# Optimization experiments

Measured on AMD Instinct MI355X. Metric: run time of the kernel, lower is better.

## Reference

```python
import jax, jax.numpy as jnp
import numpy as np

NUM_VALUES = 32000
EMB = 512
BATCH = 2048
SEQ = 64


def setup_inputs() -> dict:
    key = jax.random.key(0)
    ks = jax.random.split(key, 6)
    s = 1.0 / np.sqrt(EMB)  # torch LSTMCell init scale
    x = jax.random.randint(ks[0], (BATCH, SEQ), 0, NUM_VALUES, dtype=jnp.int64)
    emb = jax.random.normal(ks[1], (NUM_VALUES, EMB), dtype=jnp.float32)
    W_ih = jax.random.uniform(ks[2], (4 * EMB, EMB), jnp.float32, -s, s)
    W_hh = jax.random.uniform(ks[3], (4 * EMB, EMB), jnp.float32, -s, s)
    b_ih = jax.random.uniform(ks[4], (4 * EMB,), jnp.float32, -s, s)
    b_hh = jax.random.uniform(ks[5], (4 * EMB,), jnp.float32, -s, s)
    return {"x": x, "emb": emb, "W_ih": W_ih, "W_hh": W_hh, "b_ih": b_ih, "b_hh": b_hh}


def _lstm_cell(h, c, xt, W_ih, W_hh, b):
    # gates layout (torch): [i, f, g, o] along first axis of 4E
    gates = xt @ W_ih.T + h @ W_hh.T + b  # [B, 4E]
    i, f, g, o = jnp.split(gates, 4, axis=-1)
    i = jax.nn.sigmoid(i)
    f = jax.nn.sigmoid(f)
    g = jnp.tanh(g)
    o = jax.nn.sigmoid(o)
    c = f * c + i * g
    h = o * jnp.tanh(c)
    return h, c


def reference(x, emb, W_ih, W_hh, b_ih, b_hh):
    B, S = x.shape
    E = emb.shape[1]
    xe = emb[x.T]  # [S, B, E] (transpose(0,1) then embedding)
    b = b_ih + b_hh
    h0 = jnp.zeros((B, E), dtype=emb.dtype)
    c0 = jnp.zeros((B, E), dtype=emb.dtype)

    def step(carry, xt):
        h, c = carry
        h, c = _lstm_cell(h, c, xt, W_ih, W_hh, b)
        return (h, c), None

    (h, _), _ = jax.lax.scan(step, (h0, c0), xe)
    return h
```

## Files before the change

### kernel.cpp

```cpp
#include <hip/hip_runtime.h>
#include <hip/hip_bf16.h>

#define B_   2048
#define E_   512
#define S_   64
#define K_   1024
#define NG   2048

#define BM 128
#define BN 128
#define BK 64
#define ND  4

typedef __attribute__((ext_vector_type(8))) short  bfrag8;
typedef __attribute__((ext_vector_type(4))) float  f32x4;

#define WAITVM(N) asm volatile("s_waitcnt vmcnt(" #N ")" ::: "memory")
#define SBAR() do { __builtin_amdgcn_s_barrier(); __builtin_amdgcn_sched_barrier(0); } while (0)

__device__ __forceinline__ void gload16(const void* g, void* l) {
  __builtin_amdgcn_global_load_lds(
      (const __attribute__((address_space(1))) unsigned int*)g,
      (__attribute__((address_space(3))) unsigned int*)l,
      16, 0, 0);
}

__device__ __forceinline__ float sigm(float x)      { return 1.f / (1.f + __expf(-x)); }
__device__ __forceinline__ float tanh_fast(float x) { return 2.f / (1.f + __expf(-2.f * x)) - 1.f; }

__global__ __launch_bounds__(256) void prep_weights(
    const float* __restrict__ Wih, const float* __restrict__ Whh,
    const float* __restrict__ bih, const float* __restrict__ bhh,
    __hip_bfloat16* __restrict__ Wp, float* __restrict__ biasP)
{
  int p  = blockIdx.x;
  int te = p >> 7;
  int c  = p & 127;
  int hi = (c >> 6) & 1;
  int g  = (c >> 4) & 3;
  int q  = c & 15;
  int e  = te * 32 + hi * 16 + q;
  int n  = g * E_ + e;
  const float* s0 = Wih + (size_t)n * E_;
  const float* s1 = Whh + (size_t)n * E_;
  __hip_bfloat16* dst = Wp + (size_t)p * K_;
  for (int k = threadIdx.x; k < E_; k += 256) {
    dst[k]       = __float2bfloat16(s0[k]);
    dst[E_ + k]  = __float2bfloat16(s1[k]);
  }
  if (threadIdx.x == 0) biasP[p] = bih[n] + bhh[n];
}

__global__ __launch_bounds__(256) void init_state(
    const int* __restrict__ x, const float* __restrict__ emb,
    float* __restrict__ c, __hip_bfloat16* __restrict__ A0)
{
  int b  = blockIdx.x;
  int xi = x[(size_t)b * S_ + 0];
  const float* e = emb + (size_t)xi * E_;
  __hip_bfloat16* a = A0 + (size_t)b * K_;
  float* cr = c + (size_t)b * E_;
  for (int k = threadIdx.x; k < E_; k += 256) {
    a[k]       = __float2bfloat16(e[k]);
    a[E_ + k]  = __float2bfloat16(0.f);
    cr[k]      = 0.f;
  }
}

__global__ __launch_bounds__(512, 1) void lstm_step(
    const __hip_bfloat16* __restrict__ Acur,
    __hip_bfloat16* __restrict__ Anext,
    const __hip_bfloat16* __restrict__ Wp,
    const float* __restrict__ biasP,
    float* __restrict__ c,
    const int* __restrict__ x,
    const float* __restrict__ emb,
    float* __restrict__ out,
    int t)
{
  __shared__ __hip_bfloat16 As[ND][BM * BK];
  __shared__ __hip_bfloat16 Bs[ND][BN * BK];

  const int tid = threadIdx.x;
  const int x7 = blockIdx.x & 7;
  const int i  = blockIdx.x >> 3;
  const int tm = (x7 & 1) * 8 + (i & 7);
  const int te = (x7 >> 1) * 4 + (i >> 3);

  const int w  = tid >> 6, l = tid & 63;
  const int wr = w >> 1;
  const int wc = w & 1;
  const int lq = l & 15, lh = l >> 4;

  const int arow0 = tm * BM;
  const int brow0 = te * BN;
  const int e     = te * 32 + wc * 16 + lq;

  float bg[4];
#pragma unroll
  for (int n = 0; n < 4; ++n)
    bg[n] = biasP[te * 128 + wc * 64 + n * 16 + lq];

  float cold[2][4];
  int   xiv[2][4];
  const int tn = (t < S_ - 1) ? t + 1 : S_ - 1;
#pragma unroll
  for (int m = 0; m < 2; ++m)
#pragma unroll
    for (int r = 0; r < 4; ++r) {
      int b = arow0 + wr * 32 + m * 16 + lh * 4 + r;
      cold[m][r] = c[(size_t)b * E_ + e];
      xiv[m][r]  = x[(size_t)b * S_ + tn];
    }
  __builtin_amdgcn_sched_barrier(0);

  auto stageA = [&](int kt, int buf) {
    const int k0 = kt * BK;
#pragma unroll
    for (int it = 0; it < 2; ++it) {
      int ch  = it * 512 + tid;
      int cl  = ch ^ ((ch >> 3) & 7);
      int row = cl >> 3, gr = cl & 7;
      gload16(Acur + (size_t)(arow0 + row) * K_ + k0 + gr * 8, &As[buf][ch * 8]);
    }
  };
  auto stageB = [&](int kt, int buf) {
    const int k0 = kt * BK;
#pragma unroll
    for (int it = 0; it < 2; ++it) {
      int ch  = it * 512 + tid;
      int cl  = ch ^ ((ch >> 3) & 7);
      int row = cl >> 3, gr = cl & 7;
      gload16(Wp + (size_t)(brow0 + row) * K_ + k0 + gr * 8, &Bs[buf][ch * 8]);
    }
  };

  stageA(0, 0); stageB(0, 0);
  stageA(1, 1); stageB(1, 1);
  stageA(2, 2); stageB(2, 2);
  __builtin_amdgcn_sched_barrier(0);

  float ev[2][4];
#pragma unroll
  for (int m = 0; m < 2; ++m)
#pragma unroll
    for (int r = 0; r < 4; ++r)
      ev[m][r] = emb[(size_t)xiv[m][r] * E_ + e];
  __builtin_amdgcn_sched_barrier(0);

  int aoff[2][2], boff[2][4];
#pragma unroll
  for (int ks = 0; ks < 2; ++ks) {
#pragma unroll
    for (int m = 0; m < 2; ++m) {
      int cl = (wr * 32 + m * 16 + lq) * 8 + ks * 4 + lh;
      aoff[ks][m] = (cl ^ ((cl >> 3) & 7)) * 8;
    }
#pragma unroll
    for (int n = 0; n < 4; ++n) {
      int cl = (wc * 64 + n * 16 + lq) * 8 + ks * 4 + lh;
      boff[ks][n] = (cl ^ ((cl >> 3) & 7)) * 8;
    }
  }

  f32x4 acc[2][4];
#pragma unroll
  for (int m = 0; m < 2; ++m)
#pragma unroll
    for (int n = 0; n < 4; ++n)
      acc[m][n] = (f32x4){0.f, 0.f, 0.f, 0.f};

  auto mfma_iter = [&](int rb) {
    const __hip_bfloat16* Ab = &As[rb][0];
    const __hip_bfloat16* Bb = &Bs[rb][0];
#pragma unroll
    for (int ks = 0; ks < 2; ++ks) {
      bfrag8 af[2], bfr[4];
#pragma unroll
      for (int m = 0; m < 2; ++m) af[m]  = *(const bfrag8*)(Ab + aoff[ks][m]);
#pragma unroll
      for (int n = 0; n < 4; ++n) bfr[n] = *(const bfrag8*)(Bb + boff[ks][n]);
      __builtin_amdgcn_s_setprio(1);
#pragma unroll
      for (int m = 0; m < 2; ++m)
#pragma unroll
        for (int n = 0; n < 4; ++n)
          acc[m][n] = __builtin_amdgcn_mfma_f32_16x16x32_bf16(af[m], bfr[n], acc[m][n], 0, 0, 0);
      __builtin_amdgcn_s_setprio(0);
    }
  };

  WAITVM(16); SBAR(); stageA(3, 3);  stageB(3, 3);  mfma_iter(0);
  WAITVM(16); SBAR(); stageA(4, 0);  stageB(4, 0);  mfma_iter(1);
  WAITVM(16); SBAR(); stageA(5, 1);  stageB(5, 1);  mfma_iter(2);
  WAITVM(8);  SBAR(); stageA(6, 2);  stageB(6, 2);  mfma_iter(3);
#pragma unroll 1
  for (int kt = 4; kt <= 12; ++kt) {
    WAITVM(8); SBAR();
    stageA(kt + 3, (kt + 3) & 3); stageB(kt + 3, (kt + 3) & 3);
    mfma_iter(kt & 3);
  }
  WAITVM(8); SBAR(); mfma_iter(1);
  WAITVM(4); SBAR(); mfma_iter(2);
  WAITVM(0); SBAR(); mfma_iter(3);

  const bool last = (t == S_ - 1);
#pragma unroll
  for (int m = 0; m < 2; ++m) {
#pragma unroll
    for (int r = 0; r < 4; ++r) {
      int b = arow0 + wr * 32 + m * 16 + lh * 4 + r;
      float iv = acc[m][0][r] + bg[0];
      float fv = acc[m][1][r] + bg[1];
      float gv = acc[m][2][r] + bg[2];
      float ov = acc[m][3][r] + bg[3];
      size_t cidx = (size_t)b * E_ + e;
      float ig = sigm(iv), fg = sigm(fv), gg = tanh_fast(gv), og = sigm(ov);
      float cn = fg * cold[m][r] + ig * gg;
      c[cidx] = cn;
      float h = og * tanh_fast(cn);
      if (last) {
        out[cidx] = h;
      } else {
        Anext[(size_t)b * K_ + E_ + e] = __float2bfloat16(h);
        Anext[(size_t)b * K_ + e]      = __float2bfloat16(ev[m][r]);
      }
    }
  }
}

extern "C" void kernel_launch(void* const* d_in, const int* in_sizes, int n_in,
                              void* d_out, int out_size, void* d_ws, size_t ws_size,
                              hipStream_t stream) {
  const int*   x   = (const int*)d_in[0];
  const float* emb = (const float*)d_in[1];
  const float* Wih = (const float*)d_in[2];
  const float* Whh = (const float*)d_in[3];
  const float* bih = (const float*)d_in[4];
  const float* bhh = (const float*)d_in[5];
  float* out = (float*)d_out;
  (void)in_sizes; (void)n_in; (void)out_size; (void)ws_size;

  char* p = (char*)d_ws;
  __hip_bfloat16* Wp    = (__hip_bfloat16*)p;  p += (size_t)NG * K_ * 2;
  float*          biasP = (float*)p;           p += (size_t)NG * 4;
  float*          c     = (float*)p;           p += (size_t)B_ * E_ * 4;
  __hip_bfloat16* A0    = (__hip_bfloat16*)p;  p += (size_t)B_ * K_ * 2;
  __hip_bfloat16* A1    = (__hip_bfloat16*)p;  p += (size_t)B_ * K_ * 2;

  prep_weights<<<NG, 256, 0, stream>>>(Wih, Whh, bih, bhh, Wp, biasP);
  init_state<<<B_, 256, 0, stream>>>(x, emb, c, A0);
  for (int t = 0; t < S_; ++t) {
    __hip_bfloat16* Ac = (t & 1) ? A1 : A0;
    __hip_bfloat16* An = (t & 1) ? A0 : A1;
    lstm_step<<<256, 512, 0, stream>>>(Ac, An, Wp, biasP, c, x, emb, out, t);
  }
}
```

Baseline: 1.220 ms.

## Pregather all embeddings upfront and split A operand into Xe and H buffers

Replaces the per-step embedding gather (scattered fp32 loads of emb for the next timestep inside each lstm_step) with a single pregather kernel that writes all timesteps' embeddings as bf16 into a [S,B,E] buffer. The step kernel now streams its A tile from Xe for the first half of K and from a compact H buffer for the second half. Loads of bias and old cell state are moved from the prologue into the middle of the K loop to hide their latency. The cost is a 128MB workspace buffer and an extra upfront gather pass.

```diff
diff --git a/kernel.cpp b/kernel.cpp
--- a/kernel.cpp
+++ b/kernel.cpp
@@ -51,30 +51,32 @@
   if (threadIdx.x == 0) biasP[p] = bih[n] + bhh[n];
 }
 
-__global__ __launch_bounds__(256) void init_state(
+__global__ __launch_bounds__(256) void pregather(
     const int* __restrict__ x, const float* __restrict__ emb,
-    float* __restrict__ c, __hip_bfloat16* __restrict__ A0)
+    __hip_bfloat16* __restrict__ Xe)
 {
-  int b  = blockIdx.x;
-  int xi = x[(size_t)b * S_ + 0];
-  const float* e = emb + (size_t)xi * E_;
-  __hip_bfloat16* a = A0 + (size_t)b * K_;
-  float* cr = c + (size_t)b * E_;
-  for (int k = threadIdx.x; k < E_; k += 256) {
-    a[k]       = __float2bfloat16(e[k]);
-    a[E_ + k]  = __float2bfloat16(0.f);
-    cr[k]      = 0.f;
-  }
+  int row  = blockIdx.x * 4 + (threadIdx.x >> 6);
+  int lane = threadIdx.x & 63;
+  int b = row >> 6, t = row & 63;
+  size_t xi = (size_t)x[row];
+  const float* src = emb + xi * E_ + lane * 8;
+  float4 f0 = *(const float4*)(src);
+  float4 f1 = *(const float4*)(src + 4);
+  union { __hip_bfloat16 h[8]; uint4 v; } u;
+  u.h[0] = __float2bfloat16(f0.x); u.h[1] = __float2bfloat16(f0.y);
+  u.h[2] = __float2bfloat16(f0.z); u.h[3] = __float2bfloat16(f0.w);
+  u.h[4] = __float2bfloat16(f1.x); u.h[5] = __float2bfloat16(f1.y);
+  u.h[6] = __float2bfloat16(f1.z); u.h[7] = __float2bfloat16(f1.w);
+  *(uint4*)(Xe + ((size_t)t * B_ + b) * E_ + lane * 8) = u.v;
 }
 
 __global__ __launch_bounds__(512, 1) void lstm_step(
-    const __hip_bfloat16* __restrict__ Acur,
-    __hip_bfloat16* __restrict__ Anext,
+    const __hip_bfloat16* __restrict__ Xe,
+    const __hip_bfloat16* __restrict__ Hp,
+    __hip_bfloat16* __restrict__ Hn,
     const __hip_bfloat16* __restrict__ Wp,
     const float* __restrict__ biasP,
     float* __restrict__ c,
-    const int* __restrict__ x,
-    const float* __restrict__ emb,
     float* __restrict__ out,
     int t)
 {
@@ -96,36 +98,20 @@
   const int brow0 = te * BN;
   const int e     = te * 32 + wc * 16 + lq;
 
-  float bg[4];
-#pragma unroll
-  for (int n = 0; n < 4; ++n)
-    bg[n] = biasP[te * 128 + wc * 64 + n * 16 + lq];
-
-  float cold[2][4];
-  int   xiv[2][4];
-  const int tn = (t < S_ - 1) ? t + 1 : S_ - 1;
-#pragma unroll
-  for (int m = 0; m < 2; ++m)
-#pragma unroll
-    for (int r = 0; r < 4; ++r) {
-      int b = arow0 + wr * 32 + m * 16 + lh * 4 + r;
-      cold[m][r] = c[(size_t)b * E_ + e];
-      xiv[m][r]  = x[(size_t)b * S_ + tn];
-    }
-  __builtin_amdgcn_sched_barrier(0);
-
-  auto stageA = [&](int kt, int buf) {
-    const int k0 = kt * BK;
+  auto stageA = [&](int tt, int buf) {
 #pragma unroll
     for (int it = 0; it < 2; ++it) {
       int ch  = it * 512 + tid;
       int cl  = ch ^ ((ch >> 3) & 7);
       int row = cl >> 3, gr = cl & 7;
-      gload16(Acur + (size_t)(arow0 + row) * K_ + k0 + gr * 8, &As[buf][ch * 8]);
+      const __hip_bfloat16* src = (tt < 8)
+        ? Xe + ((size_t)t * B_ + arow0 + row) * E_ + tt * 64 + gr * 8
+        : Hp + (size_t)(arow0 + row) * E_ + (tt - 8) * 64 + gr * 8;
+      gload16(src, &As[buf][ch * 8]);
     }
   };
-  auto stageB = [&](int kt, int buf) {
-    const int k0 = kt * BK;
+  auto stageB = [&](int tt, int buf) {
+    const int k0 = tt * BK;
 #pragma unroll
     for (int it = 0; it < 2; ++it) {
       int ch  = it * 512 + tid;
@@ -140,14 +126,6 @@
   stageA(2, 2); stageB(2, 2);
   __builtin_amdgcn_sched_barrier(0);
 
-  float ev[2][4];
-#pragma unroll
-  for (int m = 0; m < 2; ++m)
-#pragma unroll
-    for (int r = 0; r < 4; ++r)
-      ev[m][r] = emb[(size_t)xiv[m][r] * E_ + e];
-  __builtin_amdgcn_sched_barrier(0);
-
   int aoff[2][2], boff[2][4];
 #pragma unroll
   for (int ks = 0; ks < 2; ++ks) {
@@ -190,19 +168,34 @@
     }
   };
 
-  WAITVM(16); SBAR(); stageA(3, 3);  stageB(3, 3);  mfma_iter(0);
-  WAITVM(16); SBAR(); stageA(4, 0);  stageB(4, 0);  mfma_iter(1);
-  WAITVM(16); SBAR(); stageA(5, 1);  stageB(5, 1);  mfma_iter(2);
-  WAITVM(8);  SBAR(); stageA(6, 2);  stageB(6, 2);  mfma_iter(3);
+  float bg[4];
+  float cold[2][4];
+
 #pragma unroll 1
-  for (int kt = 4; kt <= 12; ++kt) {
+  for (int kt = 0; kt < 8; ++kt) {
     WAITVM(8); SBAR();
     stageA(kt + 3, (kt + 3) & 3); stageB(kt + 3, (kt + 3) & 3);
     mfma_iter(kt & 3);
   }
-  WAITVM(8); SBAR(); mfma_iter(1);
-  WAITVM(4); SBAR(); mfma_iter(2);
-  WAITVM(0); SBAR(); mfma_iter(3);
+  WAITVM(8); SBAR();
+  stageA(11, 3); stageB(11, 3);
+#pragma unroll
+  for (int n = 0; n < 4; ++n)
+    bg[n] = biasP[te * 128 + wc * 64 + n * 16 + lq];
+#pragma unroll
+  for (int m = 0; m < 2; ++m)
+#pragma unroll
+    for (int r = 0; r < 4; ++r)
+      cold[m][r] = c[(size_t)(arow0 + wr * 32 + m * 16 + lh * 4 + r) * E_ + e];
+  __builtin_amdgcn_sched_barrier(0);
+  mfma_iter(0);
+  WAITVM(20); SBAR(); stageA(12, 0); stageB(12, 0); mfma_iter(1);
+  WAITVM(20); SBAR(); stageA(13, 1); stageB(13, 1); mfma_iter(2);
+  WAITVM(20); SBAR(); stageA(14, 2); stageB(14, 2); mfma_iter(3);
+  WAITVM(8);  SBAR(); stageA(15, 3); stageB(15, 3); mfma_iter(0);
+  WAITVM(8);  SBAR(); mfma_iter(1);
+  WAITVM(4);  SBAR(); mfma_iter(2);
+  WAITVM(0);  SBAR(); mfma_iter(3);
 
   const bool last = (t == S_ - 1);
 #pragma unroll
@@ -219,12 +212,8 @@
       float cn = fg * cold[m][r] + ig * gg;
       c[cidx] = cn;
       float h = og * tanh_fast(cn);
-      if (last) {
-        out[cidx] = h;
-      } else {
-        Anext[(size_t)b * K_ + E_ + e] = __float2bfloat16(h);
-        Anext[(size_t)b * K_ + e]      = __float2bfloat16(ev[m][r]);
-      }
+      if (last) out[cidx] = h;
+      else      Hn[cidx]  = __float2bfloat16(h);
     }
   }
 }
@@ -244,15 +233,18 @@
   char* p = (char*)d_ws;
   __hip_bfloat16* Wp    = (__hip_bfloat16*)p;  p += (size_t)NG * K_ * 2;
   float*          biasP = (float*)p;           p += (size_t)NG * 4;
+  __hip_bfloat16* Xe    = (__hip_bfloat16*)p;  p += (size_t)S_ * B_ * E_ * 2;
+  __hip_bfloat16* H0    = (__hip_bfloat16*)p;  p += (size_t)B_ * E_ * 2;
+  __hip_bfloat16* H1    = (__hip_bfloat16*)p;  p += (size_t)B_ * E_ * 2;
   float*          c     = (float*)p;           p += (size_t)B_ * E_ * 4;
-  __hip_bfloat16* A0    = (__hip_bfloat16*)p;  p += (size_t)B_ * K_ * 2;
-  __hip_bfloat16* A1    = (__hip_bfloat16*)p;  p += (size_t)B_ * K_ * 2;
 
   prep_weights<<<NG, 256, 0, stream>>>(Wih, Whh, bih, bhh, Wp, biasP);
-  init_state<<<B_, 256, 0, stream>>>(x, emb, c, A0);
+  pregather<<<(B_ * S_) / 4, 256, 0, stream>>>(x, emb, Xe);
+  hipMemsetAsync(H0, 0, (size_t)B_ * E_ * 2, stream);
+  hipMemsetAsync(c,  0, (size_t)B_ * E_ * 4, stream);
   for (int t = 0; t < S_; ++t) {
-    __hip_bfloat16* Ac = (t & 1) ? A1 : A0;
-    __hip_bfloat16* An = (t & 1) ? A0 : A1;
-    lstm_step<<<256, 512, 0, stream>>>(Ac, An, Wp, biasP, c, x, emb, out, t);
-  }
-}
+    const __hip_bfloat16* Hprev = (t & 1) ? H1 : H0;
+    __hip_bfloat16*       Hnext = (t & 1) ? H0 : H1;
+    lstm_step<<<256, 512, 0, stream>>>(Xe, Hprev, Hnext, Wp, biasP, c, out, t);
+  }
+}
```

Result: slower. 1.278 ms (+4.8%).
